# Kernel tuning notes

Measured on AMD Instinct MI355X. Metric: run time of the kernel, lower is better.

## Reference

```python
import jax, jax.numpy as jnp
import numpy as np

TEMPERATURE = 0.07
B, D = 8192, 256

def _l2norm(x, axis=-1, eps=1e-12):
    # matches torch F.normalize(p=2): x / max(||x||, eps)
    n = jnp.sqrt(jnp.sum(x * x, axis=axis, keepdims=True))
    return x / jnp.maximum(n, eps)

def setup_inputs() -> dict:
    key = jax.random.key(0)
    k1, k2, k3 = jax.random.split(key, 3)
    return {
        "h_emb": jax.random.normal(k1, (B, D), dtype=jnp.float32),
        "r_emb": jax.random.normal(k2, (B, D), dtype=jnp.float32),
        "t_emb": jax.random.normal(k3, (B, D), dtype=jnp.float32),
    }

def reference(h_emb, r_emb, t_emb):
    # query = normalize(h + r); positives/negatives = normalize(t)
    q = _l2norm(h_emb + r_emb, axis=1)          # [B, D]
    t = _l2norm(t_emb, axis=1)                  # [B, D]
    # Dense in-batch similarity. The original builds logits = [pos, off-diag negs];
    # since the diagonal of sim IS the positive similarity, cross-entropy with
    # label 0 equals logsumexp over the full row minus the diagonal entry.
    sim = jnp.einsum('bd,nd->bn', q, t) / TEMPERATURE   # [B, B]
    pos = jnp.diagonal(sim)                              # [B]
    loss = jnp.mean(jax.nn.logsumexp(sim, axis=1) - pos)
    return loss
```

## Files before the change

kernel.cpp:

```cpp
#include <hip/hip_runtime.h>
#include <hip/hip_bf16.h>

#define B_DIM 8192
#define D_DIM 256
#define GRID_GEMM 512
#define NT 16

constexpr float INV_T = 14.285714285714286f;

typedef __bf16 bf16x8 __attribute__((ext_vector_type(8)));
typedef float  f32x16 __attribute__((ext_vector_type(16)));

#define GLOBAL_U32(p) ((const __attribute__((address_space(1))) unsigned int*)(p))
#define LDS_U32(p)    ((__attribute__((address_space(3))) unsigned int*)(p))

#define WAITCNT_VM8 0x0F78

__device__ inline unsigned short f2bf(float f) {
    union { float f; unsigned u; } x; x.f = f;
    unsigned r = x.u + 0x7fffu + ((x.u >> 16) & 1u);
    return (unsigned short)(r >> 16);
}

__global__ __launch_bounds__(256) void norm_kernel(
    const float* __restrict__ h, const float* __restrict__ r,
    const float* __restrict__ t,
    unsigned short* __restrict__ qws, unsigned short* __restrict__ tws,
    float* __restrict__ rowsum, float* __restrict__ diagsum, int* __restrict__ ticket)
{
    if (blockIdx.x == 0) {
        float4* rs4 = (float4*)rowsum;
#pragma unroll
        for (int i = 0; i < 8; ++i)
            rs4[threadIdx.x * 8 + i] = make_float4(0.f, 0.f, 0.f, 0.f);
        if (threadIdx.x == 0) { *diagsum = 0.f; *ticket = 0; }
    }

    int wave = threadIdx.x >> 6;
    int lane = threadIdx.x & 63;
    int task = blockIdx.x * 4 + wave;
    bool isQ = task < B_DIM;
    int row  = isQ ? task : task - B_DIM;

    float4 v;
    if (isQ) {
        float4 a = ((const float4*)h)[row * 64 + lane];
        float4 b = ((const float4*)r)[row * 64 + lane];
        v = make_float4(a.x + b.x, a.y + b.y, a.z + b.z, a.w + b.w);
    } else {
        v = ((const float4*)t)[row * 64 + lane];
    }
    float s = v.x * v.x + v.y * v.y + v.z * v.z + v.w * v.w;
#pragma unroll
    for (int off = 32; off; off >>= 1) s += __shfl_xor(s, off, 64);
    float scale = 1.0f / fmaxf(sqrtf(s), 1e-12f);

    ushort4 o;
    o.x = f2bf(v.x * scale);
    o.y = f2bf(v.y * scale);
    o.z = f2bf(v.z * scale);
    o.w = f2bf(v.w * scale);
    ushort4* dst = (ushort4*)(isQ ? qws : tws);
    dst[row * 64 + lane] = o;
}

__global__ __launch_bounds__(256, 2) void gemm_lse_kernel(
    const unsigned char* __restrict__ qws, const unsigned char* __restrict__ tws,
    float* __restrict__ rowsum, float* __restrict__ diagsum,
    int* __restrict__ ticket, float* __restrict__ out)
{
    __shared__ __align__(16) unsigned char ldsB[4][32 * 512];
    __shared__ float wred[4];
    __shared__ int lastflag;

    const int tid  = threadIdx.x;
    const int lane = tid & 63;
    const int w    = tid >> 6;
    const int l31  = lane & 31;
    const int hi   = lane >> 5;

    const int cc   = blockIdx.x & 15;
    const int rb   = blockIdx.x >> 4;
    const int row0 = rb * 256 + w * 64;
    const int col0 = cc * 512;

    int srel[4];
#pragma unroll
    for (int it = 0; it < 4; ++it) {
        int s = it * 256 + tid;
        int n = s >> 5;
        int kc = (s & 31) ^ (n & 7);
        srel[it] = n * 512 + kc * 16;
    }

#define STAGE(snt, bufi)                                                     \
    {                                                                        \
        const unsigned char* gs = tws + (size_t)(col0 + (snt) * 32) * 512;   \
        _Pragma("unroll")                                                    \
        for (int it = 0; it < 4; ++it)                                       \
            __builtin_amdgcn_global_load_lds(                                \
                GLOBAL_U32(gs + srel[it]),                                   \
                LDS_U32(&ldsB[bufi][(it * 256 + tid) * 16]), 16, 0, 0);      \
    }

    STAGE(0, 0);
    STAGE(1, 1);

    bf16x8 a[2][16];
    {
        const unsigned char* abase = qws + (size_t)(row0 + l31) * 512 + hi * 16;
#pragma unroll
        for (int rt = 0; rt < 2; ++rt)
#pragma unroll
            for (int ks = 0; ks < 16; ++ks)
                a[rt][ks] = *(const bf16x8*)(abase + rt * (32 * 512) + ks * 32);
    }

    f32x16 rowacc[2] = {};
    float diagacc = 0.f;
    const int nsw = l31 & 7;

    for (int nt = 0; nt < NT; ++nt) {
        const int snt = (nt + 2 < NT) ? nt + 2 : NT - 1;
        STAGE(snt, (nt + 2) & 3);

        __builtin_amdgcn_s_waitcnt(WAITCNT_VM8);
        __builtin_amdgcn_s_barrier();

        const unsigned char* bbuf = ldsB[nt & 3];
        f32x16 acc0 = {}, acc1 = {};
#pragma unroll
        for (int ks = 0; ks < 16; ++ks) {
            int kc = ks * 2 + hi;
            bf16x8 b = *(const bf16x8*)(bbuf + l31 * 512 + ((kc ^ nsw) * 16));
            acc0 = __builtin_amdgcn_mfma_f32_32x32x16_bf16(a[0][ks], b, acc0, 0, 0, 0);
            acc1 = __builtin_amdgcn_mfma_f32_32x32x16_bf16(a[1][ks], b, acc1, 0, 0, 0);
        }

#pragma unroll
        for (int g = 0; g < 16; ++g) {
            rowacc[0][g] += __expf(fmaf(acc0[g], INV_T, -INV_T));
            rowacc[1][g] += __expf(fmaf(acc1[g], INV_T, -INV_T));
        }

        const int c0t = col0 + nt * 32;
        if (c0t == row0) {
#pragma unroll
            for (int g = 0; g < 16; ++g) {
                int rm = (g & 3) + 8 * (g >> 2) + 4 * hi;
                if (l31 == rm) diagacc += acc0[g] * INV_T;
            }
        }
        if (c0t == row0 + 32) {
#pragma unroll
            for (int g = 0; g < 16; ++g) {
                int rm = (g & 3) + 8 * (g >> 2) + 4 * hi;
                if (l31 == rm) diagacc += acc1[g] * INV_T;
            }
        }
    }

#pragma unroll
    for (int rt = 0; rt < 2; ++rt)
#pragma unroll
        for (int g = 0; g < 16; ++g) {
            float s = rowacc[rt][g];
            s += __shfl_xor(s, 1, 64);
            s += __shfl_xor(s, 2, 64);
            s += __shfl_xor(s, 4, 64);
            s += __shfl_xor(s, 8, 64);
            s += __shfl_xor(s, 16, 64);
            if (l31 == 0) {
                int grow = row0 + rt * 32 + (g & 3) + 8 * (g >> 2) + 4 * hi;
                atomicAdd(&rowsum[grow], s);
            }
        }

    float dsum = diagacc;
#pragma unroll
    for (int off = 32; off; off >>= 1) dsum += __shfl_xor(dsum, off, 64);
    if (lane == 0 && dsum != 0.f) atomicAdd(diagsum, dsum);

    __syncthreads();
    if (tid == 0) {
        __threadfence();
        int old = __hip_atomic_fetch_add(ticket, 1, __ATOMIC_ACQ_REL,
                                         __HIP_MEMORY_SCOPE_AGENT);
        lastflag = (old == GRID_GEMM - 1);
    }
    __syncthreads();
    if (!lastflag) return;

    float lsum = 0.f;
    for (int rr = tid; rr < B_DIM; rr += 256) {
        float rs = __hip_atomic_load(&rowsum[rr], __ATOMIC_RELAXED,
                                     __HIP_MEMORY_SCOPE_AGENT);
        lsum += __logf(rs);
    }
#pragma unroll
    for (int off = 32; off; off >>= 1) lsum += __shfl_xor(lsum, off, 64);
    if (lane == 0) wred[w] = lsum;
    __syncthreads();
    if (tid == 0) {
        float ds = __hip_atomic_load(diagsum, __ATOMIC_RELAXED,
                                     __HIP_MEMORY_SCOPE_AGENT);
        float total = wred[0] + wred[1] + wred[2] + wred[3]
                    + (float)B_DIM * INV_T
                    - ds;
        out[0] = total / (float)B_DIM;
    }
}

extern "C" void kernel_launch(void* const* d_in, const int* in_sizes, int n_in,
                              void* d_out, int out_size, void* d_ws, size_t ws_size,
                              hipStream_t stream)
{
    const float* h = (const float*)d_in[0];
    const float* r = (const float*)d_in[1];
    const float* t = (const float*)d_in[2];

    unsigned char* ws = (unsigned char*)d_ws;
    unsigned short* qws = (unsigned short*)ws;
    unsigned short* tws = (unsigned short*)(ws + 4u * 1024 * 1024);
    float* rowsum  = (float*)(ws + 8u * 1024 * 1024);
    float* diagsum = (float*)(ws + 8u * 1024 * 1024 + 32u * 1024);
    int*   ticket  = (int*)  (ws + 8u * 1024 * 1024 + 32u * 1024 + 16);

    norm_kernel<<<4096, 256, 0, stream>>>(h, r, t, qws, tws, rowsum, diagsum, ticket);
    gemm_lse_kernel<<<GRID_GEMM, 256, 0, stream>>>(
        (const unsigned char*)qws, (const unsigned char*)tws,
        rowsum, diagsum, ticket, (float*)d_out);
}
```

Before: 132.5 us.

## Fuse normalization into GEMM kernel with grid-wide arrival barrier

Merges the normalization pass into the GEMM/logsumexp kernel. Each of the 512 blocks normalizes 16 q rows and 16 t rows, then all blocks wait on a global atomic arrival counter before starting the GEMM. Zeroing of the accumulators moves to a hipMemsetAsync. This removes one kernel launch and the gap between launches. In exchange it adds a spin barrier that assumes all 512 blocks are co-resident (2 per CU), and it still needs a memset launch.

```diff
diff --git a/kernel.cpp b/kernel.cpp
--- a/kernel.cpp
+++ b/kernel.cpp
@@ -22,52 +22,13 @@
     return (unsigned short)(r >> 16);
 }
 
-__global__ __launch_bounds__(256) void norm_kernel(
+__global__ __launch_bounds__(256, 2) void fused_kernel(
     const float* __restrict__ h, const float* __restrict__ r,
     const float* __restrict__ t,
     unsigned short* __restrict__ qws, unsigned short* __restrict__ tws,
-    float* __restrict__ rowsum, float* __restrict__ diagsum, int* __restrict__ ticket)
-{
-    if (blockIdx.x == 0) {
-        float4* rs4 = (float4*)rowsum;
-#pragma unroll
-        for (int i = 0; i < 8; ++i)
-            rs4[threadIdx.x * 8 + i] = make_float4(0.f, 0.f, 0.f, 0.f);
-        if (threadIdx.x == 0) { *diagsum = 0.f; *ticket = 0; }
-    }
-
-    int wave = threadIdx.x >> 6;
-    int lane = threadIdx.x & 63;
-    int task = blockIdx.x * 4 + wave;
-    bool isQ = task < B_DIM;
-    int row  = isQ ? task : task - B_DIM;
-
-    float4 v;
-    if (isQ) {
-        float4 a = ((const float4*)h)[row * 64 + lane];
-        float4 b = ((const float4*)r)[row * 64 + lane];
-        v = make_float4(a.x + b.x, a.y + b.y, a.z + b.z, a.w + b.w);
-    } else {
-        v = ((const float4*)t)[row * 64 + lane];
-    }
-    float s = v.x * v.x + v.y * v.y + v.z * v.z + v.w * v.w;
-#pragma unroll
-    for (int off = 32; off; off >>= 1) s += __shfl_xor(s, off, 64);
-    float scale = 1.0f / fmaxf(sqrtf(s), 1e-12f);
-
-    ushort4 o;
-    o.x = f2bf(v.x * scale);
-    o.y = f2bf(v.y * scale);
-    o.z = f2bf(v.z * scale);
-    o.w = f2bf(v.w * scale);
-    ushort4* dst = (ushort4*)(isQ ? qws : tws);
-    dst[row * 64 + lane] = o;
-}
-
-__global__ __launch_bounds__(256, 2) void gemm_lse_kernel(
-    const unsigned char* __restrict__ qws, const unsigned char* __restrict__ tws,
     float* __restrict__ rowsum, float* __restrict__ diagsum,
-    int* __restrict__ ticket, float* __restrict__ out)
+    int* __restrict__ ticket, int* __restrict__ arrive,
+    float* __restrict__ out)
 {
     __shared__ __align__(16) unsigned char ldsB[4][32 * 512];
     __shared__ float wred[4];
@@ -79,6 +40,42 @@
     const int l31  = lane & 31;
     const int hi   = lane >> 5;
 
+#pragma unroll
+    for (int j = 0; j < 8; ++j) {
+        const int task = w * 8 + j;
+        const int row  = blockIdx.x * 16 + (task & 15);
+        const bool isQ = task < 16;
+        float4 v;
+        if (isQ) {
+            float4 a = ((const float4*)h)[row * 64 + lane];
+            float4 b = ((const float4*)r)[row * 64 + lane];
+            v = make_float4(a.x + b.x, a.y + b.y, a.z + b.z, a.w + b.w);
+        } else {
+            v = ((const float4*)t)[row * 64 + lane];
+        }
+        float s = v.x * v.x + v.y * v.y + v.z * v.z + v.w * v.w;
+#pragma unroll
+        for (int off = 32; off; off >>= 1) s += __shfl_xor(s, off, 64);
+        float scale = 1.0f / fmaxf(sqrtf(s), 1e-12f);
+        ushort4 o;
+        o.x = f2bf(v.x * scale);
+        o.y = f2bf(v.y * scale);
+        o.z = f2bf(v.z * scale);
+        o.w = f2bf(v.w * scale);
+        ((ushort4*)(isQ ? qws : tws))[row * 64 + lane] = o;
+    }
+
+    __syncthreads();
+    if (tid == 0) {
+        __threadfence();
+        __hip_atomic_fetch_add(arrive, 1, __ATOMIC_ACQ_REL,
+                               __HIP_MEMORY_SCOPE_AGENT);
+        while (__hip_atomic_load(arrive, __ATOMIC_ACQUIRE,
+                                 __HIP_MEMORY_SCOPE_AGENT) < GRID_GEMM)
+            __builtin_amdgcn_s_sleep(1);
+    }
+    __syncthreads();
+
     const int cc   = blockIdx.x & 15;
     const int rb   = blockIdx.x >> 4;
     const int row0 = rb * 256 + w * 64;
@@ -95,7 +92,8 @@
 
 #define STAGE(snt, bufi)                                                     \
     {                                                                        \
-        const unsigned char* gs = tws + (size_t)(col0 + (snt) * 32) * 512;   \
+        const unsigned char* gs = (const unsigned char*)tws +                \
+                                  (size_t)(col0 + (snt) * 32) * 512;         \
         _Pragma("unroll")                                                    \
         for (int it = 0; it < 4; ++it)                                       \
             __builtin_amdgcn_global_load_lds(                                \
@@ -108,7 +106,8 @@
 
     bf16x8 a[2][16];
     {
-        const unsigned char* abase = qws + (size_t)(row0 + l31) * 512 + hi * 16;
+        const unsigned char* abase =
+            (const unsigned char*)qws + (size_t)(row0 + l31) * 512 + hi * 16;
 #pragma unroll
         for (int rt = 0; rt < 2; ++rt)
 #pragma unroll
@@ -223,11 +222,12 @@
     unsigned short* qws = (unsigned short*)ws;
     unsigned short* tws = (unsigned short*)(ws + 4u * 1024 * 1024);
     float* rowsum  = (float*)(ws + 8u * 1024 * 1024);
-    float* diagsum = (float*)(ws + 8u * 1024 * 1024 + 32u * 1024);
-    int*   ticket  = (int*)  (ws + 8u * 1024 * 1024 + 32u * 1024 + 16);
-
-    norm_kernel<<<4096, 256, 0, stream>>>(h, r, t, qws, tws, rowsum, diagsum, ticket);
-    gemm_lse_kernel<<<GRID_GEMM, 256, 0, stream>>>(
-        (const unsigned char*)qws, (const unsigned char*)tws,
-        rowsum, diagsum, ticket, (float*)d_out);
+    float* diagsum = (float*)(ws + 8u * 1024 * 1024 + 32768u);
+    int*   ticket  = (int*)  (ws + 8u * 1024 * 1024 + 32768u + 4);
+    int*   arrive  = (int*)  (ws + 8u * 1024 * 1024 + 32768u + 8);
+
+    hipMemsetAsync(ws + 8u * 1024 * 1024, 0, 32768u + 16, stream);
+
+    fused_kernel<<<GRID_GEMM, 256, 0, stream>>>(
+        h, r, t, qws, tws, rowsum, diagsum, ticket, arrive, (float*)d_out);
 }
```

Result: slower. 160.1 us (+20.8%).

## Store normalized operands in MFMA fragment layout and drop LDS staging

Applied to the files above, without the earlier changes.

The norm kernel now writes the bf16 q and t rows in a tiled layout that matches the MFMA fragment order. This lets the GEMM kernel load B fragments straight from global memory (L2) with no LDS staging, barriers or waitcnt pipelining, and it removes the launch bound that asked for 2 blocks per CU. Each norm wave now processes two rows, and the accumulator zeroing moves to a hipMemsetAsync. The risk is that B reads are now direct global loads with no explicit prefetch, so memory latency may be exposed, and the memset adds an extra operation to the stream.

```diff
diff --git a/kernel.cpp b/kernel.cpp
--- a/kernel.cpp
+++ b/kernel.cpp
@@ -11,11 +11,6 @@
 typedef __bf16 bf16x8 __attribute__((ext_vector_type(8)));
 typedef float  f32x16 __attribute__((ext_vector_type(16)));
 
-#define GLOBAL_U32(p) ((const __attribute__((address_space(1))) unsigned int*)(p))
-#define LDS_U32(p)    ((__attribute__((address_space(3))) unsigned int*)(p))
-
-#define WAITCNT_VM8 0x0F78
-
 __device__ inline unsigned short f2bf(float f) {
     union { float f; unsigned u; } x; x.f = f;
     unsigned r = x.u + 0x7fffu + ((x.u >> 16) & 1u);
@@ -25,51 +20,54 @@
 __global__ __launch_bounds__(256) void norm_kernel(
     const float* __restrict__ h, const float* __restrict__ r,
     const float* __restrict__ t,
-    unsigned short* __restrict__ qws, unsigned short* __restrict__ tws,
-    float* __restrict__ rowsum, float* __restrict__ diagsum, int* __restrict__ ticket)
+    unsigned short* __restrict__ qws, unsigned short* __restrict__ tws)
 {
-    if (blockIdx.x == 0) {
-        float4* rs4 = (float4*)rowsum;
-#pragma unroll
-        for (int i = 0; i < 8; ++i)
-            rs4[threadIdx.x * 8 + i] = make_float4(0.f, 0.f, 0.f, 0.f);
-        if (threadIdx.x == 0) { *diagsum = 0.f; *ticket = 0; }
-    }
-
-    int wave = threadIdx.x >> 6;
-    int lane = threadIdx.x & 63;
-    int task = blockIdx.x * 4 + wave;
-    bool isQ = task < B_DIM;
-    int row  = isQ ? task : task - B_DIM;
-
-    float4 v;
-    if (isQ) {
-        float4 a = ((const float4*)h)[row * 64 + lane];
-        float4 b = ((const float4*)r)[row * 64 + lane];
-        v = make_float4(a.x + b.x, a.y + b.y, a.z + b.z, a.w + b.w);
-    } else {
-        v = ((const float4*)t)[row * 64 + lane];
-    }
-    float s = v.x * v.x + v.y * v.y + v.z * v.z + v.w * v.w;
-#pragma unroll
-    for (int off = 32; off; off >>= 1) s += __shfl_xor(s, off, 64);
-    float scale = 1.0f / fmaxf(sqrtf(s), 1e-12f);
-
-    ushort4 o;
-    o.x = f2bf(v.x * scale);
-    o.y = f2bf(v.y * scale);
-    o.z = f2bf(v.z * scale);
-    o.w = f2bf(v.w * scale);
+    const int lane = threadIdx.x & 63;
+    const int w    = threadIdx.x >> 6;
+    const int task0 = blockIdx.x * 8 + w * 2;
+    const bool isQ  = task0 < B_DIM;
+    const int row0  = isQ ? task0 : task0 - B_DIM;
+
+    float4 v[2];
+#pragma unroll
+    for (int j = 0; j < 2; ++j) {
+        const int row = row0 + j;
+        if (isQ) {
+            float4 a = ((const float4*)h)[row * 64 + lane];
+            float4 b = ((const float4*)r)[row * 64 + lane];
+            v[j] = make_float4(a.x + b.x, a.y + b.y, a.z + b.z, a.w + b.w);
+        } else {
+            v[j] = ((const float4*)t)[row * 64 + lane];
+        }
+    }
+    float s[2];
+#pragma unroll
+    for (int j = 0; j < 2; ++j)
+        s[j] = v[j].x * v[j].x + v[j].y * v[j].y + v[j].z * v[j].z + v[j].w * v[j].w;
+#pragma unroll
+    for (int off = 32; off; off >>= 1) {
+        s[0] += __shfl_xor(s[0], off, 64);
+        s[1] += __shfl_xor(s[1], off, 64);
+    }
     ushort4* dst = (ushort4*)(isQ ? qws : tws);
-    dst[row * 64 + lane] = o;
-}
-
-__global__ __launch_bounds__(256, 2) void gemm_lse_kernel(
+#pragma unroll
+    for (int j = 0; j < 2; ++j) {
+        const int row = row0 + j;
+        float scale = 1.0f / fmaxf(sqrtf(s[j]), 1e-12f);
+        ushort4 o;
+        o.x = f2bf(v[j].x * scale);
+        o.y = f2bf(v[j].y * scale);
+        o.z = f2bf(v[j].z * scale);
+        o.w = f2bf(v[j].w * scale);
+        dst[(row >> 5) * 2048 + (lane >> 1) * 64 + (row & 31) * 2 + (lane & 1)] = o;
+    }
+}
+
+__global__ __launch_bounds__(256) void gemm_lse_kernel(
     const unsigned char* __restrict__ qws, const unsigned char* __restrict__ tws,
     float* __restrict__ rowsum, float* __restrict__ diagsum,
     int* __restrict__ ticket, float* __restrict__ out)
 {
-    __shared__ __align__(16) unsigned char ldsB[4][32 * 512];
     __shared__ float wred[4];
     __shared__ int lastflag;
 
@@ -84,55 +82,28 @@
     const int row0 = rb * 256 + w * 64;
     const int col0 = cc * 512;
 
-    int srel[4];
-#pragma unroll
-    for (int it = 0; it < 4; ++it) {
-        int s = it * 256 + tid;
-        int n = s >> 5;
-        int kc = (s & 31) ^ (n & 7);
-        srel[it] = n * 512 + kc * 16;
-    }
-
-#define STAGE(snt, bufi)                                                     \
-    {                                                                        \
-        const unsigned char* gs = tws + (size_t)(col0 + (snt) * 32) * 512;   \
-        _Pragma("unroll")                                                    \
-        for (int it = 0; it < 4; ++it)                                       \
-            __builtin_amdgcn_global_load_lds(                                \
-                GLOBAL_U32(gs + srel[it]),                                   \
-                LDS_U32(&ldsB[bufi][(it * 256 + tid) * 16]), 16, 0, 0);      \
-    }
-
-    STAGE(0, 0);
-    STAGE(1, 1);
-
     bf16x8 a[2][16];
     {
-        const unsigned char* abase = qws + (size_t)(row0 + l31) * 512 + hi * 16;
-#pragma unroll
-        for (int rt = 0; rt < 2; ++rt)
+        const bf16x8* qa = (const bf16x8*)qws;
+#pragma unroll
+        for (int rt = 0; rt < 2; ++rt) {
+            const int pofs = ((row0 + rt * 32) >> 5) * 1024 + hi * 32 + l31;
 #pragma unroll
             for (int ks = 0; ks < 16; ++ks)
-                a[rt][ks] = *(const bf16x8*)(abase + rt * (32 * 512) + ks * 32);
+                a[rt][ks] = qa[pofs + ks * 64];
+        }
     }
 
     f32x16 rowacc[2] = {};
     float diagacc = 0.f;
-    const int nsw = l31 & 7;
+    const bf16x8* tb = (const bf16x8*)tws;
 
     for (int nt = 0; nt < NT; ++nt) {
-        const int snt = (nt + 2 < NT) ? nt + 2 : NT - 1;
-        STAGE(snt, (nt + 2) & 3);
-
-        __builtin_amdgcn_s_waitcnt(WAITCNT_VM8);
-        __builtin_amdgcn_s_barrier();
-
-        const unsigned char* bbuf = ldsB[nt & 3];
+        const int bofs = ((col0 >> 5) + nt) * 1024 + hi * 32 + l31;
         f32x16 acc0 = {}, acc1 = {};
 #pragma unroll
         for (int ks = 0; ks < 16; ++ks) {
-            int kc = ks * 2 + hi;
-            bf16x8 b = *(const bf16x8*)(bbuf + l31 * 512 + ((kc ^ nsw) * 16));
+            bf16x8 b = tb[bofs + ks * 64];
             acc0 = __builtin_amdgcn_mfma_f32_32x32x16_bf16(a[0][ks], b, acc0, 0, 0, 0);
             acc1 = __builtin_amdgcn_mfma_f32_32x32x16_bf16(a[1][ks], b, acc1, 0, 0, 0);
         }
@@ -223,10 +194,12 @@
     unsigned short* qws = (unsigned short*)ws;
     unsigned short* tws = (unsigned short*)(ws + 4u * 1024 * 1024);
     float* rowsum  = (float*)(ws + 8u * 1024 * 1024);
-    float* diagsum = (float*)(ws + 8u * 1024 * 1024 + 32u * 1024);
-    int*   ticket  = (int*)  (ws + 8u * 1024 * 1024 + 32u * 1024 + 16);
-
-    norm_kernel<<<4096, 256, 0, stream>>>(h, r, t, qws, tws, rowsum, diagsum, ticket);
+    float* diagsum = (float*)(ws + 8u * 1024 * 1024 + 32768u);
+    int*   ticket  = (int*)  (ws + 8u * 1024 * 1024 + 32768u + 4);
+
+    hipMemsetAsync(ws + 8u * 1024 * 1024, 0, 32768u + 16, stream);
+
+    norm_kernel<<<2048, 256, 0, stream>>>(h, r, t, qws, tws);
     gemm_lse_kernel<<<GRID_GEMM, 256, 0, stream>>>(
         (const unsigned char*)qws, (const unsigned char*)tws,
         rowsum, diagsum, ticket, (float*)d_out);
```

Measured after the change: 149.1 us. 1.12x slower.
